# Performance work log

Hardware: AMD Instinct MI355X
Metric: run time of the kernel (lower is better)

## Reference

```python
import jax, jax.numpy as jnp
import numpy as np

EPS = 1e-8
TEMPERATURE = 1.0


def setup_inputs() -> dict:
    key = jax.random.key(0)
    basin_seq = jax.random.normal(key, (4, 512, 64), dtype=jnp.float32)
    residual_scale = jnp.ones((), dtype=jnp.float32)  # nn.Parameter(torch.tensor(1.0))
    return {"basin_seq": basin_seq, "residual_scale": residual_scale}


def _project_to_simplex(x):
    sp = jax.nn.softplus(x)
    p = sp / (sp.sum(axis=-1, keepdims=True) + EPS)
    return jnp.maximum(p, EPS)


def _qfi_attention_weights(x, temperature):
    # x: (B, T, D)
    p = _project_to_simplex(x)
    # fisher_rao_distance_simplex re-normalizes both operands
    p = p / (p.sum(axis=-1, keepdims=True) + EPS)
    # Faithful: eps is inside the sqrt, so this is a true (B,T,T,D) reduction,
    # not sqrt(p) @ sqrt(p)^T.
    inner = jnp.sqrt(p[:, :, None, :] * p[:, None, :, :] + EPS).sum(axis=-1)  # (B,T,T)
    inner = jnp.clip(inner, -1.0 + 1e-6, 1.0 - 1e-6)
    dist = 2.0 * jnp.arccos(inner)
    logits = -dist / max(float(temperature), 1e-6)
    return jax.nn.softmax(logits, axis=-1)  # (B,T,T)


def _phi_from_activations(acts):
    # acts: (B, T, D)
    t = acts.shape[1]
    x = acts - acts.mean(axis=1, keepdims=True)
    cov = jnp.einsum('btd,bte->bde', x, x) / (t + EPS)
    var = jnp.maximum(jnp.diagonal(cov, axis1=-2, axis2=-1), EPS)  # (B,D)
    denom = jnp.maximum(jnp.sqrt(var[:, :, None] * var[:, None, :]), EPS)
    corr = jnp.clip(cov / denom, -1.0, 1.0)
    d = corr.shape[-1]
    offdiag = corr * (1.0 - jnp.eye(d, dtype=corr.dtype))
    return jnp.abs(offdiag).mean(axis=(-2, -1))  # (B,)


def _kappa_proxy(x):
    return jnp.linalg.norm(x, axis=-1).mean(axis=-1)  # (B,)


def reference(basin_seq, residual_scale):
    x = basin_seq
    for _ in range(2):
        w = _qfi_attention_weights(x, TEMPERATURE)
        x_attn = jnp.einsum('bij,bjd->bid', w, x)
        x = 0.5 * x + 0.5 * x_attn
        x = x + 0.01 * residual_scale * (x_attn - x)
    phi = _phi_from_activations(x)
    kappa = _kappa_proxy(x)
    return (x, phi, kappa)
```

## Files before the change

kernel.cpp:

```cpp
#include <hip/hip_runtime.h>
#include <math.h>

#define B_ 4
#define T_ 512
#define D_ 64
#define EPS 1e-8f

__device__ __forceinline__ float wave_sum(float v) {
#pragma unroll
  for (int m = 1; m < 64; m <<= 1) v += __shfl_xor(v, m, 64);
  return v;
}
__device__ __forceinline__ float softplus_f(float x) {
  return fmaxf(x, 0.0f) + log1pf(expf(-fabsf(x)));
}

#define DOT4(ACC, A, Bv) \
  ACC = fmaf((A).x, (Bv).x, fmaf((A).y, (Bv).y, fmaf((A).z, (Bv).z, fmaf((A).w, (Bv).w, ACC))))

__global__ __launch_bounds__(256) void proj_kernel(const float* __restrict__ x,
                                                   float* __restrict__ s) {
  int wave = threadIdx.x >> 6, lane = threadIdx.x & 63;
  int row = blockIdx.x * 4 + wave;
  float sp = softplus_f(x[row * D_ + lane]);
  float s1 = wave_sum(sp);
  float p = sp / (s1 + EPS);
  p = fmaxf(p, EPS);
  float s2 = wave_sum(p);
  s[row * D_ + lane] = sqrtf(p / (s2 + EPS));
}

__device__ __forceinline__ void stage512(const float* __restrict__ g,
                                         float* __restrict__ lds, int tid) {
#pragma unroll
  for (int h = 0; h < 2; ++h) {
    float4 v[8];
#pragma unroll
    for (int r = 0; r < 8; ++r) {
      int slot = (h * 8 + r) * 512 + tid;
      int j = slot >> 4, c4 = slot & 15;
      v[r] = *(const float4*)(g + j * 64 + ((c4 ^ ((j >> 2) & 7)) << 2));
    }
#pragma unroll
    for (int r = 0; r < 8; ++r) {
      int slot = (h * 8 + r) * 512 + tid;
      int j = slot >> 4, c4 = slot & 15;
      *(float4*)(lds + j * 64 + (c4 << 2)) = v[r];
    }
  }
}

template <int WRITE_S, int DO_COV>
__global__ __launch_bounds__(512) void fiter_kernel(
    const float* __restrict__ s_g, const float* __restrict__ x_g,
    const float* __restrict__ rsp, float* __restrict__ xout,
    float* __restrict__ sout, float* __restrict__ covp,
    float* __restrict__ meanp, float* __restrict__ diagp,
    float* __restrict__ kappap) {
  int b = blockIdx.y, i0 = blockIdx.x * 8;
  int tid = threadIdx.x;
  int w = tid >> 6, lane = tid & 63;
  const float* sb = s_g + (size_t)b * (T_ * D_);
  const float* xb = x_g + (size_t)b * (T_ * D_);

  __shared__ __align__(16) float sx[512 * 64];
  __shared__ __align__(16) float wlds[8 * 516];
  __shared__ __align__(16) float redv[8 * 68];
  __shared__ float redM[8][8];
  __shared__ float redS[8][8];
  __shared__ float t8[8][68];
  __shared__ float kred8[8];

  if (DO_COV && blockIdx.x == 0 && tid == 0) xout[B_ * T_ * D_ + b] = 0.f;

  stage512(sb, sx, tid);
  __syncthreads();

  int i4 = lane >> 4, j16 = lane & 15;
  int ia0 = i0 + 2 * i4;
  const float* A0 = sx + ia0 * 64;
  const float* A1 = A0 + 64;
  int mA0 = (ia0 >> 2) & 7, mA1 = ((ia0 + 1) >> 2) & 7;
  const float* Bp = sx + (w * 64 + 4 * j16) * 64;
  int mB = j16 & 7;

  float acc[2][4];
#pragma unroll
  for (int r = 0; r < 2; ++r)
#pragma unroll
    for (int c = 0; c < 4; ++c) acc[r][c] = 0.f;

#pragma unroll
  for (int d4 = 0; d4 < 16; ++d4) {
    float4 a0 = *(const float4*)(A0 + ((d4 ^ mA0) << 2));
    float4 a1 = *(const float4*)(A1 + ((d4 ^ mA1) << 2));
    int ob = (d4 ^ mB) << 2;
    float4 b0 = *(const float4*)(Bp + ob);
    float4 b1 = *(const float4*)(Bp + 64 + ob);
    float4 b2 = *(const float4*)(Bp + 128 + ob);
    float4 b3 = *(const float4*)(Bp + 192 + ob);
    DOT4(acc[0][0], a0, b0); DOT4(acc[0][1], a0, b1);
    DOT4(acc[0][2], a0, b2); DOT4(acc[0][3], a0, b3);
    DOT4(acc[1][0], a1, b0); DOT4(acc[1][1], a1, b1);
    DOT4(acc[1][2], a1, b2); DOT4(acc[1][3], a1, b3);
  }

  float S[2][4];
#pragma unroll
  for (int r = 0; r < 2; ++r)
#pragma unroll
    for (int c = 0; c < 4; ++c) {
      float inner = fminf(fmaxf(acc[r][c], -1.0f + 1e-6f), 1.0f - 1e-6f);
      S[r][c] = -2.0f * acosf(inner);
    }

  float m0 = fmaxf(fmaxf(S[0][0], S[0][1]), fmaxf(S[0][2], S[0][3]));
  float m1 = fmaxf(fmaxf(S[1][0], S[1][1]), fmaxf(S[1][2], S[1][3]));
#pragma unroll
  for (int mm = 1; mm < 16; mm <<= 1) {
    m0 = fmaxf(m0, __shfl_xor(m0, mm, 64));
    m1 = fmaxf(m1, __shfl_xor(m1, mm, 64));
  }
  if (j16 == 0) { redM[2 * i4][w] = m0; redM[2 * i4 + 1][w] = m1; }
  __syncthreads();

  stage512(xb, sx, tid);

  float M0 = redM[2 * i4][0], M1 = redM[2 * i4 + 1][0];
#pragma unroll
  for (int q = 1; q < 8; ++q) {
    M0 = fmaxf(M0, redM[2 * i4][q]);
    M1 = fmaxf(M1, redM[2 * i4 + 1][q]);
  }
  float e[2][4];
  float sl0 = 0.f, sl1 = 0.f;
#pragma unroll
  for (int c = 0; c < 4; ++c) {
    e[0][c] = __expf(S[0][c] - M0); sl0 += e[0][c];
    e[1][c] = __expf(S[1][c] - M1); sl1 += e[1][c];
  }
#pragma unroll
  for (int mm = 1; mm < 16; mm <<= 1) {
    sl0 += __shfl_xor(sl0, mm, 64);
    sl1 += __shfl_xor(sl1, mm, 64);
  }
  if (j16 == 0) { redS[2 * i4][w] = sl0; redS[2 * i4 + 1][w] = sl1; }
  int wb = w * 64 + 4 * j16;
#pragma unroll
  for (int r = 0; r < 2; ++r)
#pragma unroll
    for (int c = 0; c < 4; ++c) wlds[(2 * i4 + r) * 516 + wb + c] = e[r][c];
  __syncthreads();

  int js = tid & 15, dg = (tid >> 4) & 15, ig = tid >> 8;
  int xcol = ((dg ^ (js & 7)) << 2);
  float pacc[4][4];
#pragma unroll
  for (int ii = 0; ii < 4; ++ii)
#pragma unroll
    for (int k = 0; k < 4; ++k) pacc[ii][k] = 0.f;

#pragma unroll 2
  for (int jj = 0; jj < 8; ++jj) {
    int jbase = jj * 64 + js * 4;
    const float* xr = sx + jbase * 64 + xcol;
    float4 x0 = *(const float4*)(xr);
    float4 x1 = *(const float4*)(xr + 64);
    float4 x2 = *(const float4*)(xr + 128);
    float4 x3 = *(const float4*)(xr + 192);
#pragma unroll
    for (int ii = 0; ii < 4; ++ii) {
      float4 wv = *(const float4*)(wlds + (4 * ig + ii) * 516 + jbase);
      pacc[ii][0] = fmaf(wv.x, x0.x, fmaf(wv.y, x1.x, fmaf(wv.z, x2.x, fmaf(wv.w, x3.x, pacc[ii][0]))));
      pacc[ii][1] = fmaf(wv.x, x0.y, fmaf(wv.y, x1.y, fmaf(wv.z, x2.y, fmaf(wv.w, x3.y, pacc[ii][1]))));
      pacc[ii][2] = fmaf(wv.x, x0.z, fmaf(wv.y, x1.z, fmaf(wv.z, x2.z, fmaf(wv.w, x3.z, pacc[ii][2]))));
      pacc[ii][3] = fmaf(wv.x, x0.w, fmaf(wv.y, x1.w, fmaf(wv.z, x2.w, fmaf(wv.w, x3.w, pacc[ii][3]))));
    }
  }
#pragma unroll
  for (int ii = 0; ii < 4; ++ii)
#pragma unroll
    for (int k = 0; k < 4; ++k) {
      float v = pacc[ii][k];
      v += __shfl_xor(v, 1, 64);
      v += __shfl_xor(v, 2, 64);
      v += __shfl_xor(v, 4, 64);
      v += __shfl_xor(v, 8, 64);
      pacc[ii][k] = v;
    }
  if (js == 0) {
#pragma unroll
    for (int ii = 0; ii < 4; ++ii)
      *(float4*)(redv + (4 * ig + ii) * 68 + (dg << 2)) =
          make_float4(pacc[ii][0], pacc[ii][1], pacc[ii][2], pacc[ii][3]);
  }
  __syncthreads();

  {
    int row = w, d = lane;
    float ssum = 0.f;
#pragma unroll
    for (int q = 0; q < 8; ++q) ssum += redS[row][q];
    float xa = redv[row * 68 + d] / ssum;
    int ir = i0 + row;
    int mr = (ir >> 2) & 7;
    float xv = sx[ir * 64 + (((d >> 2) ^ mr) << 2) + (d & 3)];
    float c01 = 0.01f * rsp[0];
    float xn = 0.5f * (1.0f - c01) * xv + 0.5f * (1.0f + c01) * xa;
    size_t gi = ((size_t)(b * T_) + ir) * D_ + d;
    xout[gi] = xn;
    if (WRITE_S) {
      float sp = softplus_f(xn);
      float s1 = wave_sum(sp);
      float p = sp / (s1 + EPS);
      p = fmaxf(p, EPS);
      float s2 = wave_sum(p);
      sout[gi] = sqrtf(p / (s2 + EPS));
    }
    if (DO_COV) {
      t8[row][d] = xn;
      float ksq = wave_sum(xn * xn);
      if (lane == 0) kred8[row] = sqrtf(ksq);
    }
  }

  if (DO_COV) {
    __syncthreads();
    int blk = b * 64 + blockIdx.x;
    int dd = tid >> 3, e8 = tid & 7;
    float ca[8];
#pragma unroll
    for (int k = 0; k < 8; ++k) ca[k] = 0.f;
#pragma unroll
    for (int r = 0; r < 8; ++r) {
      float xd = t8[r][dd];
      float4 v0 = *(const float4*)&t8[r][e8 * 8];
      float4 v1 = *(const float4*)&t8[r][e8 * 8 + 4];
      ca[0] = fmaf(xd, v0.x, ca[0]); ca[1] = fmaf(xd, v0.y, ca[1]);
      ca[2] = fmaf(xd, v0.z, ca[2]); ca[3] = fmaf(xd, v0.w, ca[3]);
      ca[4] = fmaf(xd, v1.x, ca[4]); ca[5] = fmaf(xd, v1.y, ca[5]);
      ca[6] = fmaf(xd, v1.z, ca[6]); ca[7] = fmaf(xd, v1.w, ca[7]);
    }
    float* cp = covp + (size_t)blk * 4096 + dd * 64 + e8 * 8;
    *(float4*)(cp) = make_float4(ca[0], ca[1], ca[2], ca[3]);
    *(float4*)(cp + 4) = make_float4(ca[4], ca[5], ca[6], ca[7]);
    if (e8 == (dd >> 3)) diagp[blk * 64 + dd] = ca[dd & 7];
    if (tid < 64) {
      float ms = 0.f;
#pragma unroll
      for (int r = 0; r < 8; ++r) ms += t8[r][tid];
      meanp[blk * 64 + tid] = ms;
    }
    if (tid == 0) {
      float ks = 0.f;
#pragma unroll
      for (int r = 0; r < 8; ++r) ks += kred8[r];
      kappap[blk] = ks;
    }
  }
}

__global__ __launch_bounds__(256) void finalize_kernel(
    const float* __restrict__ covp, const float* __restrict__ meanp,
    const float* __restrict__ diagp, const float* __restrict__ kappap,
    float* __restrict__ out) {
  int g = blockIdx.x, b = blockIdx.y, tid = threadIdx.x;
  __shared__ float mred[4][64], dred[4][64];
  __shared__ float mu[64], var[64];
  __shared__ float phired[4];
  {
    int d = tid & 63, q = tid >> 6;
    float ms = 0.f, ds = 0.f;
#pragma unroll
    for (int s = 0; s < 16; ++s) {
      int sl = q * 16 + s;
      ms += meanp[(b * 64 + sl) * 64 + d];
      ds += diagp[(b * 64 + sl) * 64 + d];
    }
    mred[q][d] = ms; dred[q][d] = ds;
  }
  __syncthreads();
  if (tid < 64) {
    float m = (mred[0][tid] + mred[1][tid] + mred[2][tid] + mred[3][tid]) *
              (1.0f / 512.0f);
    float dsum = dred[0][tid] + dred[1][tid] + dred[2][tid] + dred[3][tid];
    mu[tid] = m;
    var[tid] = fmaxf(dsum * (1.0f / 512.0f) - m * m, EPS);
  }
  __syncthreads();

  int cell = g * 256 + tid;
  int dd = cell >> 6, e = cell & 63;
  float csum = 0.f;
#pragma unroll 4
  for (int s = 0; s < 64; ++s) csum += covp[(size_t)(b * 64 + s) * 4096 + cell];
  float cov = csum * (1.0f / 512.0f) - mu[dd] * mu[e];
  float psum = 0.f;
  if (e != dd) {
    float denom = fmaxf(sqrtf(var[dd] * var[e]), EPS);
    psum = fabsf(fminf(fmaxf(cov / denom, -1.0f), 1.0f));
  }
  psum = wave_sum(psum);
  if ((tid & 63) == 0) phired[tid >> 6] = psum;
  __syncthreads();
  if (tid == 0) {
    atomicAdd(&out[B_ * T_ * D_ + b],
              (phired[0] + phired[1] + phired[2] + phired[3]) * (1.0f / 4096.0f));
    if (g == 0) {
      float ks = 0.f;
#pragma unroll
      for (int s = 0; s < 64; ++s) ks += kappap[b * 64 + s];
      out[B_ * T_ * D_ + B_ + b] = ks * (1.0f / 512.0f);
    }
  }
}

extern "C" void kernel_launch(void* const* d_in, const int* in_sizes, int n_in,
                              void* d_out, int out_size, void* d_ws, size_t ws_size,
                              hipStream_t stream) {
  const float* x0 = (const float*)d_in[0];
  const float* rs = (const float*)d_in[1];
  float* out = (float*)d_out;
  float* s0    = (float*)d_ws;
  float* s1    = s0 + B_ * T_ * D_;
  float* x1    = s1 + B_ * T_ * D_;
  float* covp  = x1 + B_ * T_ * D_;
  float* meanp = covp + 256 * 4096;
  float* diagp = meanp + 256 * 64;
  float* kappap = diagp + 256 * 64;

  dim3 fgrd(64, 4);
  proj_kernel<<<(B_ * T_) / 4, 256, 0, stream>>>(x0, s0);
  fiter_kernel<1, 0><<<fgrd, 512, 0, stream>>>(s0, x0, rs, x1, s1, (float*)0,
                                               (float*)0, (float*)0, (float*)0);
  fiter_kernel<0, 1><<<fgrd, 512, 0, stream>>>(s1, x1, rs, out, (float*)0, covp,
                                               meanp, diagp, kappap);
  finalize_kernel<<<dim3(16, B_), 256, 0, stream>>>(covp, meanp, diagp, kappap,
                                                    out);
}
```

Baseline: 92.26 us.

## Use direct global-to-LDS loads and atomic covariance accumulation

Staging of the s and x tiles into LDS now uses global_load_lds direct transfers instead of round-tripping through registers. The per-block covariance, mean, diag and kappa partials are accumulated with float atomics into per-batch buffers, zeroed by the first iteration kernel, rather than written out as 256 partial tiles. The finalize kernel becomes one block per batch reading the accumulated sums. This removes a large partial-buffer write/read and the register pressure of staging, at the cost of heavy atomic contention and non-deterministic summation order.

```diff
diff --git a/kernel.cpp b/kernel.cpp
--- a/kernel.cpp
+++ b/kernel.cpp
@@ -30,33 +30,26 @@
   s[row * D_ + lane] = sqrtf(p / (s2 + EPS));
 }
 
-__device__ __forceinline__ void stage512(const float* __restrict__ g,
-                                         float* __restrict__ lds, int tid) {
-#pragma unroll
-  for (int h = 0; h < 2; ++h) {
-    float4 v[8];
-#pragma unroll
-    for (int r = 0; r < 8; ++r) {
-      int slot = (h * 8 + r) * 512 + tid;
-      int j = slot >> 4, c4 = slot & 15;
-      v[r] = *(const float4*)(g + j * 64 + ((c4 ^ ((j >> 2) & 7)) << 2));
-    }
-#pragma unroll
-    for (int r = 0; r < 8; ++r) {
-      int slot = (h * 8 + r) * 512 + tid;
-      int j = slot >> 4, c4 = slot & 15;
-      *(float4*)(lds + j * 64 + (c4 << 2)) = v[r];
-    }
-  }
-}
-
-template <int WRITE_S, int DO_COV>
+__device__ __forceinline__ void stage512_dma(const float* __restrict__ g,
+                                             float* __restrict__ lds, int tid) {
+#pragma unroll
+  for (int r = 0; r < 16; ++r) {
+    int slot = r * 512 + tid;
+    int j = slot >> 4, c4 = slot & 15;
+    const float* src = g + j * 64 + ((c4 ^ ((j >> 2) & 7)) << 2);
+    __builtin_amdgcn_global_load_lds(
+        (const __attribute__((address_space(1))) void*)src,
+        (__attribute__((address_space(3))) void*)(lds + slot * 4), 16, 0, 0);
+  }
+}
+
+template <int WRITE_S, int DO_COV, int DO_ZERO>
 __global__ __launch_bounds__(512) void fiter_kernel(
     const float* __restrict__ s_g, const float* __restrict__ x_g,
     const float* __restrict__ rsp, float* __restrict__ xout,
-    float* __restrict__ sout, float* __restrict__ covp,
-    float* __restrict__ meanp, float* __restrict__ diagp,
-    float* __restrict__ kappap) {
+    float* __restrict__ sout, float* __restrict__ covacc,
+    float* __restrict__ meanacc, float* __restrict__ diagacc,
+    float* __restrict__ kappacc) {
   int b = blockIdx.y, i0 = blockIdx.x * 8;
   int tid = threadIdx.x;
   int w = tid >> 6, lane = tid & 63;
@@ -71,9 +64,14 @@
   __shared__ float t8[8][68];
   __shared__ float kred8[8];
 
-  if (DO_COV && blockIdx.x == 0 && tid == 0) xout[B_ * T_ * D_ + b] = 0.f;
-
-  stage512(sb, sx, tid);
+  if (DO_ZERO && blockIdx.x == 0) {
+#pragma unroll
+    for (int i = 0; i < 8; ++i) covacc[b * 4096 + i * 512 + tid] = 0.f;
+    if (tid < 64) { meanacc[b * 64 + tid] = 0.f; diagacc[b * 64 + tid] = 0.f; }
+    if (tid == 0) kappacc[b] = 0.f;
+  }
+
+  stage512_dma(sb, sx, tid);
   __syncthreads();
 
   int i4 = lane >> 4, j16 = lane & 15;
@@ -124,7 +122,7 @@
   if (j16 == 0) { redM[2 * i4][w] = m0; redM[2 * i4 + 1][w] = m1; }
   __syncthreads();
 
-  stage512(xb, sx, tid);
+  stage512_dma(xb, sx, tid);
 
   float M0 = redM[2 * i4][0], M1 = redM[2 * i4 + 1][0];
 #pragma unroll
@@ -226,7 +224,6 @@
 
   if (DO_COV) {
     __syncthreads();
-    int blk = b * 64 + blockIdx.x;
     int dd = tid >> 3, e8 = tid & 7;
     float ca[8];
 #pragma unroll
@@ -241,77 +238,57 @@
       ca[4] = fmaf(xd, v1.x, ca[4]); ca[5] = fmaf(xd, v1.y, ca[5]);
       ca[6] = fmaf(xd, v1.z, ca[6]); ca[7] = fmaf(xd, v1.w, ca[7]);
     }
-    float* cp = covp + (size_t)blk * 4096 + dd * 64 + e8 * 8;
-    *(float4*)(cp) = make_float4(ca[0], ca[1], ca[2], ca[3]);
-    *(float4*)(cp + 4) = make_float4(ca[4], ca[5], ca[6], ca[7]);
-    if (e8 == (dd >> 3)) diagp[blk * 64 + dd] = ca[dd & 7];
+    float* cp = covacc + b * 4096 + dd * 64 + e8 * 8;
+#pragma unroll
+    for (int k = 0; k < 8; ++k) atomicAdd(cp + k, ca[k]);
+    if (e8 == (dd >> 3)) atomicAdd(&diagacc[b * 64 + dd], ca[dd & 7]);
     if (tid < 64) {
       float ms = 0.f;
 #pragma unroll
       for (int r = 0; r < 8; ++r) ms += t8[r][tid];
-      meanp[blk * 64 + tid] = ms;
+      atomicAdd(&meanacc[b * 64 + tid], ms);
     }
     if (tid == 0) {
       float ks = 0.f;
 #pragma unroll
       for (int r = 0; r < 8; ++r) ks += kred8[r];
-      kappap[blk] = ks;
+      atomicAdd(&kappacc[b], ks);
     }
   }
 }
 
 __global__ __launch_bounds__(256) void finalize_kernel(
-    const float* __restrict__ covp, const float* __restrict__ meanp,
-    const float* __restrict__ diagp, const float* __restrict__ kappap,
+    const float* __restrict__ covacc, const float* __restrict__ meanacc,
+    const float* __restrict__ diagacc, const float* __restrict__ kappacc,
     float* __restrict__ out) {
-  int g = blockIdx.x, b = blockIdx.y, tid = threadIdx.x;
-  __shared__ float mred[4][64], dred[4][64];
+  int b = blockIdx.x, tid = threadIdx.x;
   __shared__ float mu[64], var[64];
   __shared__ float phired[4];
-  {
-    int d = tid & 63, q = tid >> 6;
-    float ms = 0.f, ds = 0.f;
-#pragma unroll
-    for (int s = 0; s < 16; ++s) {
-      int sl = q * 16 + s;
-      ms += meanp[(b * 64 + sl) * 64 + d];
-      ds += diagp[(b * 64 + sl) * 64 + d];
-    }
-    mred[q][d] = ms; dred[q][d] = ds;
-  }
-  __syncthreads();
   if (tid < 64) {
-    float m = (mred[0][tid] + mred[1][tid] + mred[2][tid] + mred[3][tid]) *
-              (1.0f / 512.0f);
-    float dsum = dred[0][tid] + dred[1][tid] + dred[2][tid] + dred[3][tid];
+    float m = meanacc[b * 64 + tid] * (1.0f / 512.0f);
     mu[tid] = m;
-    var[tid] = fmaxf(dsum * (1.0f / 512.0f) - m * m, EPS);
-  }
-  __syncthreads();
-
-  int cell = g * 256 + tid;
-  int dd = cell >> 6, e = cell & 63;
-  float csum = 0.f;
-#pragma unroll 4
-  for (int s = 0; s < 64; ++s) csum += covp[(size_t)(b * 64 + s) * 4096 + cell];
-  float cov = csum * (1.0f / 512.0f) - mu[dd] * mu[e];
+    var[tid] = fmaxf(diagacc[b * 64 + tid] * (1.0f / 512.0f) - m * m, EPS);
+  }
+  __syncthreads();
+
   float psum = 0.f;
-  if (e != dd) {
-    float denom = fmaxf(sqrtf(var[dd] * var[e]), EPS);
-    psum = fabsf(fminf(fmaxf(cov / denom, -1.0f), 1.0f));
+#pragma unroll
+  for (int k = 0; k < 16; ++k) {
+    int cell = k * 256 + tid;
+    int dd = cell >> 6, e = cell & 63;
+    float cov = covacc[b * 4096 + cell] * (1.0f / 512.0f) - mu[dd] * mu[e];
+    if (e != dd) {
+      float denom = fmaxf(sqrtf(var[dd] * var[e]), EPS);
+      psum += fabsf(fminf(fmaxf(cov / denom, -1.0f), 1.0f));
+    }
   }
   psum = wave_sum(psum);
   if ((tid & 63) == 0) phired[tid >> 6] = psum;
   __syncthreads();
   if (tid == 0) {
-    atomicAdd(&out[B_ * T_ * D_ + b],
-              (phired[0] + phired[1] + phired[2] + phired[3]) * (1.0f / 4096.0f));
-    if (g == 0) {
-      float ks = 0.f;
-#pragma unroll
-      for (int s = 0; s < 64; ++s) ks += kappap[b * 64 + s];
-      out[B_ * T_ * D_ + B_ + b] = ks * (1.0f / 512.0f);
-    }
+    out[B_ * T_ * D_ + b] = (phired[0] + phired[1] + phired[2] + phired[3]) *
+                            (1.0f / 4096.0f);
+    out[B_ * T_ * D_ + B_ + b] = kappacc[b] * (1.0f / 512.0f);
   }
 }
 
@@ -321,20 +298,21 @@
   const float* x0 = (const float*)d_in[0];
   const float* rs = (const float*)d_in[1];
   float* out = (float*)d_out;
-  float* s0    = (float*)d_ws;
-  float* s1    = s0 + B_ * T_ * D_;
-  float* x1    = s1 + B_ * T_ * D_;
-  float* covp  = x1 + B_ * T_ * D_;
-  float* meanp = covp + 256 * 4096;
-  float* diagp = meanp + 256 * 64;
-  float* kappap = diagp + 256 * 64;
+  float* s0     = (float*)d_ws;
+  float* s1     = s0 + B_ * T_ * D_;
+  float* x1     = s1 + B_ * T_ * D_;
+  float* covacc = x1 + B_ * T_ * D_;
+  float* meanacc = covacc + B_ * 4096;
+  float* diagacc = meanacc + B_ * 64;
+  float* kappacc = diagacc + B_ * 64;
 
   dim3 fgrd(64, 4);
   proj_kernel<<<(B_ * T_) / 4, 256, 0, stream>>>(x0, s0);
-  fiter_kernel<1, 0><<<fgrd, 512, 0, stream>>>(s0, x0, rs, x1, s1, (float*)0,
-                                               (float*)0, (float*)0, (float*)0);
-  fiter_kernel<0, 1><<<fgrd, 512, 0, stream>>>(s1, x1, rs, out, (float*)0, covp,
-                                               meanp, diagp, kappap);
-  finalize_kernel<<<dim3(16, B_), 256, 0, stream>>>(covp, meanp, diagp, kappap,
-                                                    out);
-}
+  fiter_kernel<1, 0, 1><<<fgrd, 512, 0, stream>>>(s0, x0, rs, x1, s1, covacc,
+                                                  meanacc, diagacc, kappacc);
+  fiter_kernel<0, 1, 0><<<fgrd, 512, 0, stream>>>(s1, x1, rs, out, (float*)0,
+                                                  covacc, meanacc, diagacc,
+                                                  kappacc);
+  finalize_kernel<<<B_, 256, 0, stream>>>(covacc, meanacc, diagacc, kappacc,
+                                          out);
+}
```

New measurement: 139.4 us. +51.1%, slower.
